# Performance work log

Measured on AMD Instinct MI355X. Metric: run time of the kernel, lower is better.

## Reference

```python
import jax, jax.numpy as jnp
import numpy as np
from jax import lax

V, E, H, L1, L2, NL = 32000, 512, 1024, 1024, 1024, 2
TX, TY = 2048, 512


def setup_inputs() -> dict:
    key = jax.random.key(0)
    ks = iter(jax.random.split(key, 24))
    s = 0.05
    f = lambda shape: (jax.random.normal(next(ks), shape, dtype=jnp.float32) * s)
    inp = {
        'x': jax.random.randint(next(ks), (TX,), 0, V),
        'y': jax.random.randint(next(ks), (TY,), 0, V),
        'emb': f((V, E)),
        # encoder LSTM (2 layers); bias = b_ih + b_hh folded into one vector (same math)
        'enc_Wih0': f((4 * H, E)), 'enc_Whh0': f((4 * H, H)), 'enc_b0': f((4 * H,)),
        'enc_Wih1': f((4 * H, H)), 'enc_Whh1': f((4 * H, H)), 'enc_b1': f((4 * H,)),
        'fc1_w': f((L1, H)), 'fc1_b': f((L1,)),
        'fc2_w': f((L2, L1)), 'fc2_b': f((L2,)),
        # decoder LSTM: layer0 input_size=1 (scalar token id cast to float)
        'dec_Wih0': f((4 * L2, 1)), 'dec_Whh0': f((4 * L2, L2)), 'dec_b0': f((4 * L2,)),
        'dec_Wih1': f((4 * L2, L2)), 'dec_Whh1': f((4 * L2, L2)), 'dec_b1': f((4 * L2,)),
        'out_w': f((V, L2)), 'out_b': f((V,)),
    }
    return inp


def _lstm_cell(x_in, h, c, Wih, Whh, b):
    g = Wih @ x_in + Whh @ h + b              # (4H,)
    i, fg, gg, o = jnp.split(g, 4)
    i = jax.nn.sigmoid(i); fg = jax.nn.sigmoid(fg)
    gg = jnp.tanh(gg); o = jax.nn.sigmoid(o)
    c = fg * c + i * gg
    return o * jnp.tanh(c), c


def _lstm_layer(xs, Wih, Whh, b):
    Hd = Whh.shape[1]
    def step(carry, xt):
        h, c = carry
        h, c = _lstm_cell(xt, h, c, Wih, Whh, b)
        return (h, c), h
    (h, _), ys = lax.scan(step, (jnp.zeros((Hd,), xs.dtype), jnp.zeros((Hd,), xs.dtype)), xs)
    return ys, h


def reference(x, y, emb,
              enc_Wih0, enc_Whh0, enc_b0, enc_Wih1, enc_Whh1, enc_b1,
              fc1_w, fc1_b, fc2_w, fc2_b,
              dec_Wih0, dec_Whh0, dec_b0, dec_Wih1, dec_Whh1, dec_b1,
              out_w, out_b):
    # ---- Encoder ----
    xe = emb[x]                                   # (TX, E)
    ys0, _ = _lstm_layer(xe, enc_Wih0, enc_Whh0, enc_b0)
    _, h_last = _lstm_layer(ys0, enc_Wih1, enc_Whh1, enc_b1)   # h of top layer
    f1 = jax.nn.relu(fc1_w @ h_last + fc1_b)
    f2 = jax.nn.relu(fc2_w @ f1 + fc2_b)          # (L2,)
    h_init = jnp.stack([f2] * NL)                 # (NL, L2); used for both h and c

    def dec_step(carry, _):
        xt, hs, cs = carry                        # xt scalar float32
        h0, c0 = _lstm_cell(xt[None], hs[0], cs[0], dec_Wih0, dec_Whh0, dec_b0)
        h1, c1 = _lstm_cell(h0, hs[1], cs[1], dec_Wih1, dec_Whh1, dec_b1)
        logits = out_w @ h1 + out_b               # (V,)
        best = jnp.argmax(logits).astype(jnp.float32)
        return (best, jnp.stack([h0, h1]), jnp.stack([c0, c1])), logits

    x0 = y[0].astype(jnp.float32)
    carry0 = (x0, h_init, h_init)
    _, logits_seq = lax.scan(dec_step, carry0, None, length=TY - 1)  # (TY-1, V)
    outputs = jnp.concatenate([jnp.zeros((1, V), jnp.float32), logits_seq], axis=0)
    return jax.nn.log_softmax(outputs, axis=1)    # eval-mode output
```

## Files before the change

### kernel.cpp

```cpp
#include <hip/hip_runtime.h>
#include <cmath>

#define NV 32000
#define NE 512
#define NH 1024
#define NTX 2048
#define NTY 512
#define NWG 256
#define TPB 512

#define ENC_PH ((unsigned)(NTX + 3))

typedef float vf4 __attribute__((ext_vector_type(4)));
typedef unsigned uv4 __attribute__((ext_vector_type(4)));
typedef unsigned long long u64;
typedef unsigned long long uv2 __attribute__((ext_vector_type(2)));

__device__ inline float sigm(float x){ return 1.0f/(1.0f + expf(-x)); }

__device__ inline float wred(float v){
  #pragma unroll
  for (int m = 32; m; m >>= 1) v += __shfl_xor(v, m, 64);
  return v;
}

__device__ inline void sto(float* p, float v){
  __hip_atomic_store(p, v, __ATOMIC_RELAXED, __HIP_MEMORY_SCOPE_AGENT);
}

__device__ inline void cohv16(const float* base, vf4* h){
  const float* p = base + (threadIdx.x & 63)*4;
  asm volatile(
    "global_load_dwordx4 %0, %4, off sc0 sc1\n\t"
    "global_load_dwordx4 %1, %4, off offset:1024 sc0 sc1\n\t"
    "global_load_dwordx4 %2, %4, off offset:2048 sc0 sc1\n\t"
    "global_load_dwordx4 %3, %4, off offset:3072 sc0 sc1\n\t"
    "s_waitcnt vmcnt(0)"
    : "=&v"(h[0]), "=&v"(h[1]), "=&v"(h[2]), "=&v"(h[3])
    : "v"(p) : "memory");
}

__device__ inline void cohp4(const u64* base, u64* d){
  const u64* p = base + (threadIdx.x & 63)*4;
  uv2 a, b;
  asm volatile(
    "global_load_dwordx4 %0, %2, off sc0 sc1\n\t"
    "global_load_dwordx4 %1, %2, off offset:16 sc0 sc1\n\t"
    "s_waitcnt vmcnt(0)"
    : "=&v"(a), "=&v"(b) : "v"(p) : "memory");
  d[0] = a[0]; d[1] = a[1]; d[2] = b[0]; d[3] = b[1];
}

__device__ inline void gbar(unsigned* flags, unsigned ph){
  __syncthreads();
  if (threadIdx.x == 0)
    __hip_atomic_store(&flags[blockIdx.x], ph, __ATOMIC_RELEASE, __HIP_MEMORY_SCOPE_AGENT);
  if (threadIdx.x < 64){
    const unsigned* p = flags + threadIdx.x*4;
    for (;;){
      uv4 f;
      asm volatile("global_load_dwordx4 %0, %1, off sc0 sc1\n\ts_waitcnt vmcnt(0)"
                   : "=&v"(f) : "v"(p) : "memory");
      if (__all((int)(f[0] >= ph && f[1] >= ph && f[2] >= ph && f[3] >= ph))) break;
      __builtin_amdgcn_s_sleep(2);
    }
  }
  __syncthreads();
}


__global__ __launch_bounds__(TPB, 2) void enc_kernel(
    const int* __restrict__ x, const float* __restrict__ emb,
    const float* __restrict__ Wih0, const float* __restrict__ Whh0, const float* __restrict__ b0,
    const float* __restrict__ Wih1, const float* __restrict__ Whh1, const float* __restrict__ b1,
    const float* __restrict__ fc1w, const float* __restrict__ fc1b,
    const float* __restrict__ fc2w, const float* __restrict__ fc2b,
    char* __restrict__ ws)
{
  unsigned* flags = (unsigned*)ws;
  float* h0buf = (float*)(ws + 1024);
  float* h1buf = h0buf + 2048;
  float* ysbuf = h1buf + 2048;
  float* f1buf = ysbuf + 2048;
  float* f2buf = f1buf + 1024;

  const int tid = threadIdx.x, wg = blockIdx.x;
  const int wid = tid >> 6, lane = tid & 63;
  const bool isA = (wid < 4);
  const int j = wg*4 + (wid & 3);
  unsigned ph = 0;

  vf4 wa[4][4], wb[4][4];
  float bias[4];
  if (isA){
    #pragma unroll
    for (int g = 0; g < 4; ++g){
      const float* r = Whh0 + (size_t)(j + g*1024)*1024 + lane*4;
      #pragma unroll
      for (int q = 0; q < 4; ++q) wa[g][q] = *(const vf4*)(r + q*256);
      const float* r2 = Wih0 + (size_t)(j + g*1024)*512 + lane*4;
      wb[g][0] = *(const vf4*)(r2);
      wb[g][1] = *(const vf4*)(r2 + 256);
      wb[g][2] = vf4{0.f,0.f,0.f,0.f};
      wb[g][3] = vf4{0.f,0.f,0.f,0.f};
      bias[g] = b0[j + g*1024];
    }
  } else {
    #pragma unroll
    for (int g = 0; g < 4; ++g){
      const float* r = Wih1 + (size_t)(j + g*1024)*1024 + lane*4;
      const float* r2 = Whh1 + (size_t)(j + g*1024)*1024 + lane*4;
      #pragma unroll
      for (int q = 0; q < 4; ++q){
        wa[g][q] = *(const vf4*)(r + q*256);
        wb[g][q] = *(const vf4*)(r2 + q*256);
      }
      bias[g] = b1[j + g*1024];
    }
  }

  float c = 0.f;
  if (lane == 0){
    if (isA) sto(&h0buf[j], 0.f);
    else     sto(&h1buf[j], 0.f);
  }
  ph++; gbar(flags, ph);

  vf4 xe[2] = { vf4{0,0,0,0}, vf4{0,0,0,0} };
  if (isA){
    const float* e = emb + (size_t)x[0]*NE + lane*4;
    xe[0] = *(const vf4*)e;
    xe[1] = *(const vf4*)(e + 256);
  }

  for (int t = 0; t <= NTX; ++t){
    if (isA){
      if (t < NTX){
        vf4 hs[4]; cohv16(h0buf + (t&1)*1024, hs);
        vf4 xc[2] = { xe[0], xe[1] };
        if (t + 1 < NTX){
          const float* e = emb + (size_t)x[t+1]*NE + lane*4;
          xe[0] = *(const vf4*)e;
          xe[1] = *(const vf4*)(e + 256);
        }
        float p[4];
        #pragma unroll
        for (int g = 0; g < 4; ++g){
          vf4 acc = wa[g][0]*hs[0];
          acc += wa[g][1]*hs[1];
          acc += wa[g][2]*hs[2];
          acc += wa[g][3]*hs[3];
          acc += wb[g][0]*xc[0];
          acc += wb[g][1]*xc[1];
          p[g] = acc.x + acc.y + acc.z + acc.w;
        }
        #pragma unroll
        for (int g = 0; g < 4; ++g) p[g] = wred(p[g]) + bias[g];
        float ig = sigm(p[0]), fg = sigm(p[1]), gg = tanhf(p[2]), og = sigm(p[3]);
        c = fg*c + ig*gg;
        float hn = og * tanhf(c);
        if (lane == 0){
          sto(&h0buf[((t&1)^1)*1024 + j], hn);
          sto(&ysbuf[(t&1)*1024 + j], hn);
        }
      }
    } else {
      if (t >= 1){
        const int t1 = t - 1;
        vf4 ys[4]; cohv16(ysbuf + (t1&1)*1024, ys);
        vf4 hs[4]; cohv16(h1buf + (t1&1)*1024, hs);
        float p[4];
        #pragma unroll
        for (int g = 0; g < 4; ++g){
          vf4 acc = wa[g][0]*ys[0];
          acc += wa[g][1]*ys[1];
          acc += wa[g][2]*ys[2];
          acc += wa[g][3]*ys[3];
          acc += wb[g][0]*hs[0];
          acc += wb[g][1]*hs[1];
          acc += wb[g][2]*hs[2];
          acc += wb[g][3]*hs[3];
          p[g] = acc.x + acc.y + acc.z + acc.w;
        }
        #pragma unroll
        for (int g = 0; g < 4; ++g) p[g] = wred(p[g]) + bias[g];
        float ig = sigm(p[0]), fg = sigm(p[1]), gg = tanhf(p[2]), og = sigm(p[3]);
        c = fg*c + ig*gg;
        float hn = og * tanhf(c);
        if (lane == 0) sto(&h1buf[((t1&1)^1)*1024 + j], hn);
      }
    }
    ph++; gbar(flags, ph);
  }

  if (isA){
    vf4 hs[4]; cohv16(h1buf, hs);
    const float* r = fc1w + (size_t)j*1024 + lane*4;
    vf4 acc = (*(const vf4*)(r      ))*hs[0];
    acc    += (*(const vf4*)(r + 256))*hs[1];
    acc    += (*(const vf4*)(r + 512))*hs[2];
    acc    += (*(const vf4*)(r + 768))*hs[3];
    float s = wred(acc.x + acc.y + acc.z + acc.w) + fc1b[j];
    if (lane == 0) sto(&f1buf[j], fmaxf(s, 0.f));
  }
  ph++; gbar(flags, ph);
  if (isA){
    vf4 fs[4]; cohv16(f1buf, fs);
    const float* r = fc2w + (size_t)j*1024 + lane*4;
    vf4 acc = (*(const vf4*)(r      ))*fs[0];
    acc    += (*(const vf4*)(r + 256))*fs[1];
    acc    += (*(const vf4*)(r + 512))*fs[2];
    acc    += (*(const vf4*)(r + 768))*fs[3];
    float s = wred(acc.x + acc.y + acc.z + acc.w) + fc2b[j];
    if (lane == 0) sto(&f2buf[j], fmaxf(s, 0.f));
  }
}

__global__ __launch_bounds__(TPB, 2) void dec_kernel(
    const int* __restrict__ y,
    const float* __restrict__ dWih0, const float* __restrict__ dWhh0, const float* __restrict__ db0,
    const float* __restrict__ dWih1, const float* __restrict__ dWhh1, const float* __restrict__ db1,
    const float* __restrict__ out_w, const float* __restrict__ out_b,
    float* __restrict__ out, char* __restrict__ ws)
{
  unsigned* flags = (unsigned*)ws;
  float* h0buf = (float*)(ws + 1024);
  float* h1buf = h0buf + 2048;
  float* f2buf = h1buf + 2048 + 2048 + 1024;
  u64* parts   = (u64*)(ws + 33792);

  const int tid = threadIdx.x, wg = blockIdx.x;
  const int wid = tid >> 6, lane = tid & 63;
  const bool isA = (wid < 4);
  const int j = wg*4 + (wid & 3);
  unsigned ph = ENC_PH;

  vf4 wa[4][4], wb[4][4];
  float bias[4], wx[4];
  if (isA){
    #pragma unroll
    for (int g = 0; g < 4; ++g){
      const float* r = dWhh0 + (size_t)(j + g*1024)*1024 + lane*4;
      #pragma unroll
      for (int q = 0; q < 4; ++q) wa[g][q] = *(const vf4*)(r + q*256);
      wx[g]   = dWih0[j + g*1024];
      bias[g] = db0[j + g*1024];
    }
  } else {
    #pragma unroll
    for (int g = 0; g < 4; ++g){
      const float* r = dWih1 + (size_t)(j + g*1024)*1024 + lane*4;
      const float* r2 = dWhh1 + (size_t)(j + g*1024)*1024 + lane*4;
      #pragma unroll
      for (int q = 0; q < 4; ++q){
        wa[g][q] = *(const vf4*)(r + q*256);
        wb[g][q] = *(const vf4*)(r2 + q*256);
      }
      bias[g] = db1[j + g*1024];
      wx[g] = 0.f;
    }
  }

  float c = f2buf[j];
  if (lane == 0){
    if (isA) sto(&h0buf[j], c);
    else     sto(&h1buf[j], c);
  }
  const float y0f = (float)y[0];
  ph++; gbar(flags, ph);

  __shared__ u64 sbest[8];

  for (int s = 0; s < NTY - 1; ++s){
    const int rp = s & 1, wp = rp ^ 1;

    if (isA){
      float xt;
      if (s == 0) xt = y0f;
      else {
        u64 q4[4]; cohp4(parts, q4);
        u64 b = q4[0];
        if (q4[1] > b) b = q4[1];
        if (q4[2] > b) b = q4[2];
        if (q4[3] > b) b = q4[3];
        #pragma unroll
        for (int m = 32; m; m >>= 1){
          u64 v = __shfl_xor(b, m, 64);
          if (v > b) b = v;
        }
        unsigned row = ~(unsigned)(b & 0xFFFFFFFFull);
        xt = (float)row;
      }
      vf4 hs[4]; cohv16(h0buf + rp*1024, hs);
      float p[4];
      #pragma unroll
      for (int g = 0; g < 4; ++g){
        vf4 acc = wa[g][0]*hs[0];
        acc += wa[g][1]*hs[1];
        acc += wa[g][2]*hs[2];
        acc += wa[g][3]*hs[3];
        p[g] = acc.x + acc.y + acc.z + acc.w;
      }
      #pragma unroll
      for (int g = 0; g < 4; ++g) p[g] = wred(p[g]) + wx[g]*xt + bias[g];
      float ig = sigm(p[0]), fg = sigm(p[1]), gg = tanhf(p[2]), og = sigm(p[3]);
      c = fg*c + ig*gg;
      float hn = og * tanhf(c);
      if (lane == 0) sto(&h0buf[wp*1024 + j], hn);
    }
    ph++; gbar(flags, ph);

    if (!isA){
      vf4 u[4];  cohv16(h0buf + wp*1024, u);
      vf4 hs[4]; cohv16(h1buf + rp*1024, hs);
      float p[4];
      #pragma unroll
      for (int g = 0; g < 4; ++g){
        vf4 acc = wa[g][0]*u[0];
        acc += wa[g][1]*u[1];
        acc += wa[g][2]*u[2];
        acc += wa[g][3]*u[3];
        acc += wb[g][0]*hs[0];
        acc += wb[g][1]*hs[1];
        acc += wb[g][2]*hs[2];
        acc += wb[g][3]*hs[3];
        p[g] = acc.x + acc.y + acc.z + acc.w;
      }
      #pragma unroll
      for (int g = 0; g < 4; ++g) p[g] = wred(p[g]) + bias[g];
      float ig = sigm(p[0]), fg = sigm(p[1]), gg = tanhf(p[2]), og = sigm(p[3]);
      c = fg*c + ig*gg;
      float hn = og * tanhf(c);
      if (lane == 0) sto(&h1buf[wp*1024 + j], hn);
    }
    ph++; gbar(flags, ph);

    {
      vf4 hv[4]; cohv16(h1buf + wp*1024, hv);
      u64 best = 0ull;
      float* orow = out + (size_t)(s + 1)*NV;
      for (int idx = wid; idx < 125; idx += 8){
        const int row = wg*125 + idx;
        const float* r = out_w + (size_t)row*1024 + lane*4;
        vf4 acc = (*(const vf4*)(r      ))*hv[0];
        acc    += (*(const vf4*)(r + 256))*hv[1];
        acc    += (*(const vf4*)(r + 512))*hv[2];
        acc    += (*(const vf4*)(r + 768))*hv[3];
        float pp = wred(acc.x + acc.y + acc.z + acc.w);
        float logit = pp + out_b[row];
        if (lane == 0) orow[row] = logit;
        unsigned bbits = __float_as_uint(logit);
        unsigned key = bbits ^ ((unsigned)(((int)bbits) >> 31) | 0x80000000u);
        u64 pk = ((u64)key << 32) | (u64)(unsigned)(~row);
        if (pk > best) best = pk;
      }
      if (lane == 0) sbest[wid] = best;
      __syncthreads();
      if (tid == 0){
        u64 m = sbest[0];
        #pragma unroll
        for (int q = 1; q < 8; ++q) if (sbest[q] > m) m = sbest[q];
        __hip_atomic_store(&parts[wg], m, __ATOMIC_RELAXED, __HIP_MEMORY_SCOPE_AGENT);
      }
    }
    ph++; gbar(flags, ph);
  }
}

__global__ void lsm_kernel(float* __restrict__ out){
  __shared__ float red[256];
  const int row = blockIdx.x, tid = threadIdx.x;
  float* r = out + (size_t)row*NV;
  if (row == 0){
    const float v = -logf((float)NV);
    for (int i = tid; i < NV; i += 256) r[i] = v;
    return;
  }
  float m = -1e30f;
  for (int i = tid; i < NV; i += 256) m = fmaxf(m, r[i]);
  red[tid] = m; __syncthreads();
  for (int st = 128; st; st >>= 1){ if (tid < st) red[tid] = fmaxf(red[tid], red[tid+st]); __syncthreads(); }
  m = red[0]; __syncthreads();
  float s = 0.f;
  for (int i = tid; i < NV; i += 256) s += expf(r[i] - m);
  red[tid] = s; __syncthreads();
  for (int st = 128; st; st >>= 1){ if (tid < st) red[tid] += red[tid+st]; __syncthreads(); }
  const float lse = m + logf(red[0]);
  __syncthreads();
  for (int i = tid; i < NV; i += 256) r[i] -= lse;
}

extern "C" void kernel_launch(void* const* d_in, const int* in_sizes, int n_in,
                              void* d_out, int out_size, void* d_ws, size_t ws_size,
                              hipStream_t stream)
{
  (void)in_sizes; (void)n_in; (void)out_size; (void)ws_size;
  const int*   x     = (const int*)  d_in[0];
  const int*   y     = (const int*)  d_in[1];
  const float* emb   = (const float*)d_in[2];
  const float* eWih0 = (const float*)d_in[3];
  const float* eWhh0 = (const float*)d_in[4];
  const float* eb0   = (const float*)d_in[5];
  const float* eWih1 = (const float*)d_in[6];
  const float* eWhh1 = (const float*)d_in[7];
  const float* eb1   = (const float*)d_in[8];
  const float* fc1w  = (const float*)d_in[9];
  const float* fc1b  = (const float*)d_in[10];
  const float* fc2w  = (const float*)d_in[11];
  const float* fc2b  = (const float*)d_in[12];
  const float* dWih0 = (const float*)d_in[13];
  const float* dWhh0 = (const float*)d_in[14];
  const float* db0   = (const float*)d_in[15];
  const float* dWih1 = (const float*)d_in[16];
  const float* dWhh1 = (const float*)d_in[17];
  const float* db1   = (const float*)d_in[18];
  const float* out_w = (const float*)d_in[19];
  const float* out_b = (const float*)d_in[20];
  float* out = (float*)d_out;
  char* ws = (char*)d_ws;

  hipMemsetAsync(ws, 0, 1024, stream);
  enc_kernel<<<dim3(NWG), dim3(TPB), 0, stream>>>(x, emb, eWih0, eWhh0, eb0,
                                                  eWih1, eWhh1, eb1,
                                                  fc1w, fc1b, fc2w, fc2b, ws);
  dec_kernel<<<dim3(NWG), dim3(TPB), 0, stream>>>(y, dWih0, dWhh0, db0,
                                                  dWih1, dWhh1, db1,
                                                  out_w, out_b, out, ws);
  lsm_kernel<<<dim3(NTY), dim3(256), 0, stream>>>(out);
}
```

Baseline: 35.08 ms.

## Use byte-packed barrier flags and stage shared hidden states in LDS

The grid barrier now stores one byte flag per workgroup and polls a single dword per lane with modular phase comparison and no sleep, shrinking the poll footprint and latency. The decoder moves to 1024-thread workgroups, where dedicated spare waves prefetch h0/h1 into LDS so the compute waves read from shared memory instead of coherent global loads. The output projection is spread across 16 waves. This adds LDS use, register pressure from launch_bounds(1024,4), and depends on the 8-bit phase wrap being correct.

New measurement: 43.84 ms. 1.25x slower.

```diff
diff --git a/kernel.cpp b/kernel.cpp
--- a/kernel.cpp
+++ b/kernel.cpp
@@ -8,6 +8,7 @@
 #define NTY 512
 #define NWG 256
 #define TPB 512
+#define DTPB 1024
 
 #define ENC_PH ((unsigned)(NTX + 3))
 
@@ -51,18 +52,28 @@
   d[0] = a[0]; d[1] = a[1]; d[2] = b[0]; d[3] = b[1];
 }
 
-__device__ inline void gbar(unsigned* flags, unsigned ph){
+__device__ inline void gbar(unsigned char* flags, unsigned ph){
   __syncthreads();
-  if (threadIdx.x == 0)
-    __hip_atomic_store(&flags[blockIdx.x], ph, __ATOMIC_RELEASE, __HIP_MEMORY_SCOPE_AGENT);
+  if (threadIdx.x == 0){
+    unsigned v = ph & 0xFFu;
+    asm volatile("s_waitcnt vmcnt(0)\n\t"
+                 "global_store_byte %0, %1, off sc0 sc1"
+                 :: "v"(flags + blockIdx.x), "v"(v) : "memory");
+  }
   if (threadIdx.x < 64){
-    const unsigned* p = flags + threadIdx.x*4;
+    const unsigned* p = (const unsigned*)flags + (threadIdx.x & 63);
+    const unsigned ph8 = ph & 0xFFu;
     for (;;){
-      uv4 f;
-      asm volatile("global_load_dwordx4 %0, %1, off sc0 sc1\n\ts_waitcnt vmcnt(0)"
-                   : "=&v"(f) : "v"(p) : "memory");
-      if (__all((int)(f[0] >= ph && f[1] >= ph && f[2] >= ph && f[3] >= ph))) break;
-      __builtin_amdgcn_s_sleep(2);
+      unsigned w;
+      asm volatile("global_load_dword %0, %1, off sc0 sc1\n\ts_waitcnt vmcnt(0)"
+                   : "=v"(w) : "v"(p) : "memory");
+      unsigned ok = 1u;
+      #pragma unroll
+      for (int k = 0; k < 4; ++k){
+        unsigned f = (w >> (8*k)) & 0xFFu;
+        ok &= (((f - ph8) & 0xFFu) <= 1u) ? 1u : 0u;
+      }
+      if (__all((int)ok)) break;
     }
   }
   __syncthreads();
@@ -77,7 +88,7 @@
     const float* __restrict__ fc2w, const float* __restrict__ fc2b,
     char* __restrict__ ws)
 {
-  unsigned* flags = (unsigned*)ws;
+  unsigned char* flags = (unsigned char*)ws;
   float* h0buf = (float*)(ws + 1024);
   float* h1buf = h0buf + 2048;
   float* ysbuf = h1buf + 2048;
@@ -216,14 +227,14 @@
   }
 }
 
-__global__ __launch_bounds__(TPB, 2) void dec_kernel(
+__global__ __launch_bounds__(DTPB, 4) void dec_kernel(
     const int* __restrict__ y,
     const float* __restrict__ dWih0, const float* __restrict__ dWhh0, const float* __restrict__ db0,
     const float* __restrict__ dWih1, const float* __restrict__ dWhh1, const float* __restrict__ db1,
     const float* __restrict__ out_w, const float* __restrict__ out_b,
     float* __restrict__ out, char* __restrict__ ws)
 {
-  unsigned* flags = (unsigned*)ws;
+  unsigned char* flags = (unsigned char*)ws;
   float* h0buf = (float*)(ws + 1024);
   float* h1buf = h0buf + 2048;
   float* f2buf = h1buf + 2048 + 2048 + 1024;
@@ -232,8 +243,14 @@
   const int tid = threadIdx.x, wg = blockIdx.x;
   const int wid = tid >> 6, lane = tid & 63;
   const bool isA = (wid < 4);
+  const bool isB = (wid >= 4 && wid < 8);
   const int j = wg*4 + (wid & 3);
   unsigned ph = ENC_PH;
+
+  __shared__ float h1stage[1024];
+  __shared__ float h0stage[1024];
+  __shared__ float chstage[1024];
+  __shared__ u64 sbest[16];
 
   vf4 wa[4][4], wb[4][4];
   float bias[4], wx[4];
@@ -246,7 +263,7 @@
       wx[g]   = dWih0[j + g*1024];
       bias[g] = db0[j + g*1024];
     }
-  } else {
+  } else if (isB){
     #pragma unroll
     for (int g = 0; g < 4; ++g){
       const float* r = dWih1 + (size_t)(j + g*1024)*1024 + lane*4;
@@ -263,13 +280,11 @@
 
   float c = f2buf[j];
   if (lane == 0){
-    if (isA) sto(&h0buf[j], c);
-    else     sto(&h1buf[j], c);
+    if (isA)      sto(&h0buf[j], c);
+    else if (isB) sto(&h1buf[j], c);
   }
   const float y0f = (float)y[0];
   ph++; gbar(flags, ph);
-
-  __shared__ u64 sbest[8];
 
   for (int s = 0; s < NTY - 1; ++s){
     const int rp = s & 1, wp = rp ^ 1;
@@ -291,7 +306,13 @@
         unsigned row = ~(unsigned)(b & 0xFFFFFFFFull);
         xt = (float)row;
       }
-      vf4 hs[4]; cohv16(h0buf + rp*1024, hs);
+      vf4 hs[4];
+      if (s == 0){
+        cohv16(h0buf + rp*1024, hs);
+      } else {
+        #pragma unroll
+        for (int q = 0; q < 4; ++q) hs[q] = *(const vf4*)&h0stage[q*256 + lane*4];
+      }
       float p[4];
       #pragma unroll
       for (int g = 0; g < 4; ++g){
@@ -307,12 +328,18 @@
       c = fg*c + ig*gg;
       float hn = og * tanhf(c);
       if (lane == 0) sto(&h0buf[wp*1024 + j], hn);
+    } else if (wid == 8){
+      vf4 hv[4]; cohv16(h1buf + rp*1024, hv);
+      #pragma unroll
+      for (int q = 0; q < 4; ++q) *(vf4*)&h1stage[q*256 + lane*4] = hv[q];
     }
     ph++; gbar(flags, ph);
 
-    if (!isA){
+    if (isB){
       vf4 u[4];  cohv16(h0buf + wp*1024, u);
-      vf4 hs[4]; cohv16(h1buf + rp*1024, hs);
+      vf4 hs[4];
+      #pragma unroll
+      for (int q = 0; q < 4; ++q) hs[q] = *(const vf4*)&h1stage[q*256 + lane*4];
       float p[4];
       #pragma unroll
       for (int g = 0; g < 4; ++g){
@@ -335,11 +362,23 @@
     }
     ph++; gbar(flags, ph);
 
+    if (wid == 15){
+      vf4 hv[4]; cohv16(h1buf + wp*1024, hv);
+      #pragma unroll
+      for (int q = 0; q < 4; ++q) *(vf4*)&chstage[q*256 + lane*4] = hv[q];
+    } else if (wid == 14){
+      vf4 hv[4]; cohv16(h0buf + wp*1024, hv);
+      #pragma unroll
+      for (int q = 0; q < 4; ++q) *(vf4*)&h0stage[q*256 + lane*4] = hv[q];
+    }
+    __syncthreads();
     {
-      vf4 hv[4]; cohv16(h1buf + wp*1024, hv);
+      vf4 hv[4];
+      #pragma unroll
+      for (int q = 0; q < 4; ++q) hv[q] = *(const vf4*)&chstage[q*256 + lane*4];
       u64 best = 0ull;
       float* orow = out + (size_t)(s + 1)*NV;
-      for (int idx = wid; idx < 125; idx += 8){
+      for (int idx = wid; idx < 125; idx += 16){
         const int row = wg*125 + idx;
         const float* r = out_w + (size_t)row*1024 + lane*4;
         vf4 acc = (*(const vf4*)(r      ))*hv[0];
@@ -359,7 +398,7 @@
       if (tid == 0){
         u64 m = sbest[0];
         #pragma unroll
-        for (int q = 1; q < 8; ++q) if (sbest[q] > m) m = sbest[q];
+        for (int q = 1; q < 16; ++q) if (sbest[q] > m) m = sbest[q];
         __hip_atomic_store(&parts[wg], m, __ATOMIC_RELAXED, __HIP_MEMORY_SCOPE_AGENT);
       }
     }
@@ -423,8 +462,8 @@
   enc_kernel<<<dim3(NWG), dim3(TPB), 0, stream>>>(x, emb, eWih0, eWhh0, eb0,
                                                   eWih1, eWhh1, eb1,
                                                   fc1w, fc1b, fc2w, fc2b, ws);
-  dec_kernel<<<dim3(NWG), dim3(TPB), 0, stream>>>(y, dWih0, dWhh0, db0,
-                                                  dWih1, dWhh1, db1,
-                                                  out_w, out_b, out, ws);
+  dec_kernel<<<dim3(NWG), dim3(DTPB), 0, stream>>>(y, dWih0, dWhh0, db0,
+                                                   dWih1, dWhh1, db1,
+                                                   out_w, out_b, out, ws);
   lsm_kernel<<<dim3(NTY), dim3(256), 0, stream>>>(out);
 }
```
